# Kernel tuning notes

Hardware: AMD Instinct MI355X
Metric: run time of the kernel (lower is better)

The kernel has to match this reference:

```python
import jax, jax.numpy as jnp
import numpy as np

B, D, E = 8, 256, 2048
H, DK, DV = 8, 32, 32
LN_EPS = 1e-6
MASK_FILL = -1e9


def setup_inputs() -> dict:
    key = jax.random.key(0)
    ks = jax.random.split(key, 6)
    scale = 1.0 / np.sqrt(D)
    x = jax.random.normal(ks[0], (B, D, E), dtype=jnp.float32)
    mask = jax.random.randint(ks[1], (B, E, E), 0, 2).astype(bool)
    w_qs = jax.random.normal(ks[2], (D, H * DK), dtype=jnp.float32) * scale
    w_ks = jax.random.normal(ks[3], (D, H * DK), dtype=jnp.float32) * scale
    w_vs = jax.random.normal(ks[4], (D, H * DV), dtype=jnp.float32) * scale
    w_fc = jax.random.normal(ks[5], (H * DV, D), dtype=jnp.float32) * scale
    ln_gamma = jnp.ones((D,), dtype=jnp.float32)
    ln_beta = jnp.zeros((D,), dtype=jnp.float32)
    return {"x": x, "mask": mask, "w_qs": w_qs, "w_ks": w_ks,
            "w_vs": w_vs, "w_fc": w_fc, "ln_gamma": ln_gamma, "ln_beta": ln_beta}


def reference(x, mask, w_qs, w_ks, w_vs, w_fc, ln_gamma, ln_beta):
    # x: [B, D, E] -> s: [B, E, D]  (edges as sequence, features as d_model)
    s = jnp.transpose(x, (0, 2, 1))
    residual = s
    # LayerNorm applied to queries only (as in the original MultiHeadAttention)
    mu = jnp.mean(s, axis=-1, keepdims=True)
    var = jnp.mean((s - mu) ** 2, axis=-1, keepdims=True)
    q_in = (s - mu) * jax.lax.rsqrt(var + LN_EPS) * ln_gamma + ln_beta
    # projections -> [B, H, E, dk/dv]
    q = (q_in @ w_qs).reshape(B, E, H, DK).transpose(0, 2, 1, 3)
    k = (s @ w_ks).reshape(B, E, H, DK).transpose(0, 2, 1, 3)
    v = (s @ w_vs).reshape(B, E, H, DV).transpose(0, 2, 1, 3)
    temperature = jnp.sqrt(jnp.asarray(DK, dtype=q.dtype))
    scores = jnp.einsum('bhqd,bhkd->bhqk', q / temperature, k)
    scores = jnp.where(mask[:, None, :, :], scores, MASK_FILL)
    attn = jax.nn.softmax(scores, axis=-1)  # [B, H, E, E]
    out = jnp.einsum('bhqk,bhkd->bhqd', attn, v)
    out = out.transpose(0, 2, 1, 3).reshape(B, E, H * DV)
    out = out @ w_fc + residual  # dropout is identity in eval mode
    x_out = jnp.transpose(out, (0, 2, 1))  # back to [B, D, E]
    # attention-per-edge diagnostic (no gradient in original: attn.detach())
    attn_d = jax.lax.stop_gradient(attn)
    m = mask[:, None, :, :].astype(attn.dtype)  # [B, 1, E, E]
    attn_per_edge = jnp.sum(attn_d * m, axis=(1, 2)) / jnp.sum(m, axis=(1, 2))
    return (x_out, attn, attn_per_edge)
```

## Files before the change

kernel.cpp:

```cpp
#include <hip/hip_runtime.h>
#include <hip/hip_fp16.h>

#define TB 8
#define TD 256
#define TE 2048
#define TH 8

typedef _Float16 h8 __attribute__((ext_vector_type(8)));
typedef _Float16 h2_t __attribute__((ext_vector_type(2)));
typedef float    f4 __attribute__((ext_vector_type(4)));

static __device__ __forceinline__ unsigned int packh2(float a, float b){
  __half2 h = __floats2half2_rn(a, b);
  return __builtin_bit_cast(unsigned int, h);
}
static __device__ __forceinline__ h2_t u2h(unsigned int u){
  return __builtin_bit_cast(h2_t, u);
}
static __device__ __forceinline__ float fdot2f(h2_t a, h2_t b, float c){
#if __has_builtin(__builtin_amdgcn_fdot2)
  return __builtin_amdgcn_fdot2(a, b, c, false);
#else
  return c + (float)a[0]*(float)b[0] + (float)a[1]*(float)b[1];
#endif
}

__global__ __launch_bounds__(256) void k_pack(const unsigned int* __restrict__ mraw,
                       unsigned int* __restrict__ packed, float* __restrict__ num){
  __shared__ int oks;
  const int t = threadIdx.x;
  if(t == 0) oks = 1;
  __syncthreads();
  int ok = 1;
  for(int i=t; i<4096; i+=256) if(mraw[i] > 1u) ok = 0;
  if(!ok) atomicAnd(&oks, 0);
  __syncthreads();
  const int isInt = oks;

  const int row = blockIdx.x*4 + (t >> 6);
  const int w = t & 63;
  const size_t base = (size_t)row*TE + (size_t)w*32;
  unsigned int bits = 0;
  if(isInt){
    const unsigned int* p = mraw + base;
    #pragma unroll
    for(int j=0;j<32;j++) bits |= (p[j] & 1u) << j;
  } else {
    const unsigned char* p = (const unsigned char*)mraw + base;
    #pragma unroll
    for(int j=0;j<32;j++) bits |= (unsigned int)(p[j] != 0) << j;
  }
  packed[(size_t)row*64 + w] = bits;
  if(blockIdx.x < 64) num[blockIdx.x*256 + t] = 0.f;
}

__global__ __launch_bounds__(256) void k_denom(const unsigned int* __restrict__ packed,
                        float* __restrict__ denom){
  const int b = blockIdx.z;
  const int k = blockIdx.x*256 + threadIdx.x;
  const int q0 = blockIdx.y*64;
  const unsigned int* p = packed + ((size_t)b*TE + q0)*64 + (k >> 5);
  const unsigned sh = k & 31;
  int cnt = 0;
  #pragma unroll 8
  for(int q=0;q<64;q++) cnt += (p[(size_t)q*64] >> sh) & 1u;
  atomicAdd(&denom[b*TE + k], (float)cnt);
}

__global__ __launch_bounds__(256) void k_wpack(
    const float* __restrict__ wqs, const float* __restrict__ wks,
    const float* __restrict__ wvs, const float* __restrict__ wfc,
    unsigned int* __restrict__ wq2, unsigned int* __restrict__ wk2,
    unsigned int* __restrict__ wv2, unsigned int* __restrict__ wf2){
  const int idx = blockIdx.x*256 + threadIdx.x;
  const int m = idx >> 15;
  const int r = idx & 32767;
  const int dd2 = r >> 8, cc = r & 255;
  const float* src = (m==0) ? wqs : (m==1) ? wks : (m==2) ? wvs : wfc;
  unsigned int* dst = (m==0) ? wq2 : (m==1) ? wk2 : (m==2) ? wv2 : wf2;
  dst[dd2*256 + cc] = packh2(src[(2*dd2)*256 + cc], src[(2*dd2+1)*256 + cc]);
}

__global__ __launch_bounds__(256) void k_qkv(
    const float* __restrict__ x,
    const unsigned int* __restrict__ wq2, const unsigned int* __restrict__ wk2,
    const unsigned int* __restrict__ wv2,
    const float* __restrict__ gamma, const float* __restrict__ beta,
    _Float16* __restrict__ qh, _Float16* __restrict__ kh, _Float16* __restrict__ vt){
  __shared__ float xs[16][260];
  __shared__ unsigned int qi2[16][132];
  __shared__ unsigned int xs2[16][132];
  __shared__ float mu_s[16], rs_s[16];
  const int t = threadIdx.x;
  const int b = blockIdx.y;
  const int e0 = blockIdx.x*16;

  for(int i=t;i<16*256;i+=256){
    int el = i & 15, dd = i >> 4;
    xs[el][dd] = x[((size_t)(b*TD + dd))*TE + e0 + el];
  }
  __syncthreads();
  {
    int row = t >> 4, j = t & 15;
    float s1=0.f, s2=0.f;
    #pragma unroll
    for(int i=0;i<16;i++){ float v = xs[row][j*16+i]; s1 += v; s2 += v*v; }
    #pragma unroll
    for(int off=1; off<16; off<<=1){ s1 += __shfl_xor(s1, off); s2 += __shfl_xor(s2, off); }
    if(j==0){
      float m = s1 * (1.f/256.f);
      float var = s2 * (1.f/256.f) - m*m;
      mu_s[row] = m;
      rs_s[row] = rsqrtf(var + 1e-6f);
    }
  }
  __syncthreads();
  for(int i=t;i<16*128;i+=256){
    int r = i >> 7, dd2 = i & 127;
    float x0 = xs[r][2*dd2], x1 = xs[r][2*dd2+1];
    xs2[r][dd2] = packh2(x0, x1);
    float q0v = (x0 - mu_s[r]) * rs_s[r] * gamma[2*dd2]   + beta[2*dd2];
    float q1v = (x1 - mu_s[r]) * rs_s[r] * gamma[2*dd2+1] + beta[2*dd2+1];
    qi2[r][dd2] = packh2(q0v, q1v);
  }
  __syncthreads();

  const int c = t;
  float aq[16], ak[16], av[16];
  #pragma unroll
  for(int r=0;r<16;r++){ aq[r]=0.f; ak[r]=0.f; av[r]=0.f; }
  for(int dd2=0; dd2<128; dd2+=4){
    unsigned int wq[4], wk[4], wv[4];
    #pragma unroll
    for(int u=0;u<4;u++){
      wq[u] = wq2[(dd2+u)*256 + c];
      wk[u] = wk2[(dd2+u)*256 + c];
      wv[u] = wv2[(dd2+u)*256 + c];
    }
    #pragma unroll
    for(int r=0;r<16;r++){
      uint4 a4 = *(const uint4*)&qi2[r][dd2];
      uint4 s4 = *(const uint4*)&xs2[r][dd2];
      aq[r] = fdot2f(u2h(a4.x), u2h(wq[0]), aq[r]);
      aq[r] = fdot2f(u2h(a4.y), u2h(wq[1]), aq[r]);
      aq[r] = fdot2f(u2h(a4.z), u2h(wq[2]), aq[r]);
      aq[r] = fdot2f(u2h(a4.w), u2h(wq[3]), aq[r]);
      ak[r] = fdot2f(u2h(s4.x), u2h(wk[0]), ak[r]);
      ak[r] = fdot2f(u2h(s4.y), u2h(wk[1]), ak[r]);
      ak[r] = fdot2f(u2h(s4.z), u2h(wk[2]), ak[r]);
      ak[r] = fdot2f(u2h(s4.w), u2h(wk[3]), ak[r]);
      av[r] = fdot2f(u2h(s4.x), u2h(wv[0]), av[r]);
      av[r] = fdot2f(u2h(s4.y), u2h(wv[1]), av[r]);
      av[r] = fdot2f(u2h(s4.z), u2h(wv[2]), av[r]);
      av[r] = fdot2f(u2h(s4.w), u2h(wv[3]), av[r]);
    }
  }
  const int hh = c >> 5, d2 = c & 31;
  const float scl = 0.17677669529663687f;
  const size_t hb = ((size_t)(b*TH + hh))*TE;
  #pragma unroll
  for(int r=0;r<16;r++){
    size_t idx = (hb + e0 + r)*32 + d2;
    qh[idx] = (_Float16)(aq[r]*scl);
    kh[idx] = (_Float16)(ak[r]);
  }
  unsigned int pk[8];
  #pragma unroll
  for(int i2=0;i2<8;i2++) pk[i2] = packh2(av[2*i2], av[2*i2+1]);
  const int jj = (e0 >> 4) & 1;
  _Float16* vr = vt + ((size_t)(b*TH + hh)*32 + d2)*TE + (e0 & ~31) + 4*jj;
  #pragma unroll
  for(int gp=0; gp<4; gp++){
    uint2 w2v; w2v.x = pk[2*gp]; w2v.y = pk[2*gp+1];
    *(uint2*)&vr[8*gp] = w2v;
  }
}

__global__ __launch_bounds__(256) void k_attn(
    const _Float16* __restrict__ qh, const _Float16* __restrict__ kh, const _Float16* __restrict__ vt,
    const unsigned int* __restrict__ packed,
    float* __restrict__ attn, _Float16* __restrict__ owh, float* __restrict__ num){
  __shared__ unsigned int mb[64][66];
  __shared__ float num_s[TE];
  __shared__ __align__(16) f4 S4[4][272];

  const int t = threadIdx.x;
  int bid = blockIdx.x;
  bid = (bid & 7) * 256 + (bid >> 3);
  const int qt = bid & 31;
  const int bhid = bid >> 5;
  const int h = bhid & 7, b = bhid >> 3;
  const size_t bh = (size_t)bhid * TE;
  const _Float16* Qg = qh + bh*32;
  const _Float16* Kg = kh + bh*32;
  const _Float16* Vg = vt + bh*32;
  const int q0 = qt*64;

  const int wid = t >> 6, l = t & 63, g = l >> 4, c = l & 15;
  const int qr = wid*16 + c;
  const f4 f4z = {0.f, 0.f, 0.f, 0.f};

  for(int i=t;i<TE;i+=256) num_s[i] = 0.f;
  for(int i=t;i<64*64;i+=256){
    int r = i >> 6, w = i & 63;
    mb[r][w] = packed[((size_t)b*TE + q0 + r)*64 + w];
  }
  __syncthreads();

  const h8 qf = *(const h8*)(Qg + (size_t)(q0 + qr)*32 + g*8);
  const unsigned int* mrow = mb[qr];

  float ll = 0.f;
  for(int kt=0; kt<32; ++kt){
    h8 kf[4];
    #pragma unroll
    for(int j=0;j<4;j++) kf[j] = *(const h8*)(Kg + (size_t)(kt*64 + j*16 + c)*32 + g*8);
    f4 s[4];
    #pragma unroll
    for(int j=0;j<4;j++) s[j] = __builtin_amdgcn_mfma_f32_16x16x32_f16(kf[j], qf, f4z, 0, 0, 0);
    const unsigned mw0 = mrow[kt*2], mw1 = mrow[kt*2+1];
    #pragma unroll
    for(int j=0;j<4;j++){
      const unsigned mw = (j>>1) ? mw1 : mw0;
      #pragma unroll
      for(int r=0;r<4;r++){
        float sv = ((mw >> ((j&1)*16 + 4*g + r)) & 1u) ? s[j][r] : -1e9f;
        ll += __expf(sv);
      }
    }
  }
  ll += __shfl_xor(ll, 16);
  ll += __shfl_xor(ll, 32);
  const float rl = 1.f / ll;

  f4 oacc[2] = {f4z, f4z};
  f4* Sw = S4[wid];
  float* abase = attn + (bh + q0 + wid*16)*TE;
  for(int kt=0; kt<32; ++kt){
    h8 kf[4];
    #pragma unroll
    for(int j=0;j<4;j++) kf[j] = *(const h8*)(Kg + (size_t)(kt*64 + j*16 + c)*32 + g*8);
    f4 s[4];
    #pragma unroll
    for(int j=0;j<4;j++) s[j] = __builtin_amdgcn_mfma_f32_16x16x32_f16(kf[j], qf, f4z, 0, 0, 0);
    const unsigned mw0 = mrow[kt*2], mw1 = mrow[kt*2+1];
    unsigned int pk[4][2];
    #pragma unroll
    for(int j=0;j<4;j++){
      const unsigned mw = (j>>1) ? mw1 : mw0;
      f4 p;
      #pragma unroll
      for(int r=0;r<4;r++){
        float sv = ((mw >> ((j&1)*16 + 4*g + r)) & 1u) ? s[j][r] : -1e9f;
        p[r] = __expf(sv) * rl;
      }
      Sw[c*17 + 4*j + g] = p;
      pk[j][0] = packh2(p[0], p[1]);
      pk[j][1] = packh2(p[2], p[3]);
    }
    #pragma unroll
    for(int kc=0;kc<2;kc++){
      uint4 pu = {pk[2*kc][0], pk[2*kc][1], pk[2*kc+1][0], pk[2*kc+1][1]};
      h8 pf = __builtin_bit_cast(h8, pu);
      #pragma unroll
      for(int du=0;du<2;du++){
        h8 vf = *(const h8*)(Vg + (size_t)(du*16 + c)*TE + kt*64 + kc*32 + g*8);
        oacc[du] = __builtin_amdgcn_mfma_f32_16x16x32_f16(vf, pf, oacc[du], 0, 0, 0);
      }
    }
    f4 v[4];
    #pragma unroll
    for(int u=0;u<4;u++) v[u] = Sw[(u*4+g)*17 + c];
    #pragma unroll
    for(int u=0;u<4;u++)
      __builtin_nontemporal_store(v[u], (f4*)(abase + (size_t)(u*4+g)*TE + kt*64 + c*4));
    f4 a = v[0] + v[1] + v[2] + v[3];
    #pragma unroll
    for(int q=0;q<4;q++){ a[q] += __shfl_xor(a[q], 16); a[q] += __shfl_xor(a[q], 32); }
    if(l < 16){
      float* np = &num_s[kt*64 + c*4];
      atomicAdd(np+0, a[0]); atomicAdd(np+1, a[1]);
      atomicAdd(np+2, a[2]); atomicAdd(np+3, a[3]);
    }
  }

  #pragma unroll
  for(int du=0;du<2;du++){
    uint2 ov;
    ov.x = packh2(oacc[du][0], oacc[du][1]);
    ov.y = packh2(oacc[du][2], oacc[du][3]);
    *(uint2*)&owh[((size_t)b*TE + q0 + qr)*256 + h*32 + du*16 + 4*g] = ov;
  }
  __syncthreads();
  for(int i=t;i<TE;i+=256) atomicAdd(&num[(size_t)b*TE + i], num_s[i]);
}

__global__ __launch_bounds__(256) void k_fc(
    const _Float16* __restrict__ owh, const unsigned int* __restrict__ wf2,
    const float* __restrict__ x, float* __restrict__ xout){
  __shared__ unsigned int os2[16][132];
  __shared__ float xt[16][260];
  const int t = threadIdx.x;
  const int b = blockIdx.y;
  const int e0 = blockIdx.x * 16;
  const unsigned int* ow2 = (const unsigned int*)owh;
  for(int i=t;i<16*128;i+=256){
    int r = i >> 7, dd2 = i & 127;
    os2[r][dd2] = ow2[((size_t)b*TE + e0 + r)*128 + dd2];
  }
  for(int i=t;i<4096;i+=256){
    int el = i & 15, dd = i >> 4;
    xt[el][dd] = x[((size_t)(b*TD + dd))*TE + e0 + el];
  }
  __syncthreads();
  const int c = t;
  float f[16];
  #pragma unroll
  for(int r=0;r<16;r++) f[r] = 0.f;
  for(int dd2=0; dd2<128; dd2+=4){
    unsigned int wf[4];
    #pragma unroll
    for(int u=0;u<4;u++) wf[u] = wf2[(dd2+u)*256 + c];
    #pragma unroll
    for(int r=0;r<16;r++){
      uint4 o4 = *(const uint4*)&os2[r][dd2];
      f[r] = fdot2f(u2h(o4.x), u2h(wf[0]), f[r]);
      f[r] = fdot2f(u2h(o4.y), u2h(wf[1]), f[r]);
      f[r] = fdot2f(u2h(o4.z), u2h(wf[2]), f[r]);
      f[r] = fdot2f(u2h(o4.w), u2h(wf[3]), f[r]);
    }
  }
  __syncthreads();
  #pragma unroll
  for(int r=0;r<16;r++) xt[r][c] = f[r] + xt[r][c];
  __syncthreads();
  for(int i=t;i<4096;i+=256){
    int el = i & 15, dd = i >> 4;
    xout[((size_t)(b*TD + dd))*TE + e0 + el] = xt[el][dd];
  }
}

__global__ void k_edge(const float* __restrict__ num, const float* __restrict__ denom,
                       float* __restrict__ pe){
  int idx = blockIdx.x*256 + threadIdx.x;
  pe[idx] = num[idx] / (8.f * denom[idx]);
}

extern "C" void kernel_launch(void* const* d_in, const int* in_sizes, int n_in,
                              void* d_out, int out_size, void* d_ws, size_t ws_size,
                              hipStream_t stream){
  const float* x   = (const float*)d_in[0];
  const unsigned int* mraw = (const unsigned int*)d_in[1];
  const float* wqs = (const float*)d_in[2];
  const float* wks = (const float*)d_in[3];
  const float* wvs = (const float*)d_in[4];
  const float* wfc = (const float*)d_in[5];
  const float* gamma = (const float*)d_in[6];
  const float* beta  = (const float*)d_in[7];

  float* xout = (float*)d_out;
  float* attn = xout + (size_t)TB*TD*TE;
  float* pe   = attn + (size_t)TB*TH*TE*TE;

  const size_t SZ = (size_t)TB*TH*TE*32;
  _Float16* qhp = (_Float16*)((char*)d_ws + 256);
  _Float16* khp = qhp + SZ;
  _Float16* vtp = khp + SZ;
  _Float16* owh = vtp + SZ;
  unsigned int* packed = (unsigned int*)(owh + SZ);
  float* num   = (float*)(packed + (size_t)TB*TE*64);
  float* denom = num + (size_t)TB*TE;
  unsigned int* wq2 = (unsigned int*)(denom + (size_t)TB*TE);
  unsigned int* wk2 = wq2 + 32768;
  unsigned int* wv2 = wk2 + 32768;
  unsigned int* wf2 = wv2 + 32768;

  hipMemsetAsync(denom, 0, (size_t)TB*TE*sizeof(float), stream);
  k_wpack<<<512, 256, 0, stream>>>(wqs, wks, wvs, wfc, wq2, wk2, wv2, wf2);
  k_pack<<<TB*TE/4, 256, 0, stream>>>(mraw, packed, num);
  k_denom<<<dim3(TE/256, TE/64, TB), 256, 0, stream>>>(packed, denom);
  k_qkv<<<dim3(TE/16, TB), 256, 0, stream>>>(x, wq2, wk2, wv2, gamma, beta, qhp, khp, vtp);
  k_attn<<<TB*TH*TE/64, 256, 0, stream>>>(qhp, khp, vtp, packed, attn, owh, num);
  k_fc<<<dim3(TE/16, TB), 256, 0, stream>>>(owh, wf2, x, xout);
  k_edge<<<TB*TE/256, 256, 0, stream>>>(num, denom, pe);
}
```

Baseline: 413.5 us.

## Use MFMA for QKV and FC projections, fold log2e into Q scale, drop mask LDS staging

The QKV and output projections move from fdot2 scalar loops to 16x16x32 f16 MFMA, using transposed fp16 weight buffers built by the weight-pack kernel. The Q scale now includes log2(e), so the attention kernel can use exp2f instead of __expf. The attention kernel also reads mask bits straight from global memory as uint2 rather than staging them in shared memory. The projections were a small share of total time, so the benefit is limited, and the scattered per-element V stores may be less efficient than before.

Result: slower. 447.0 us (+8.1%).

```diff
diff --git a/kernel.cpp b/kernel.cpp
--- a/kernel.cpp
+++ b/kernel.cpp
@@ -1,5 +1,6 @@
 #include <hip/hip_runtime.h>
 #include <hip/hip_fp16.h>
+#include <math.h>
 
 #define TB 8
 #define TD 256
@@ -7,22 +8,11 @@
 #define TH 8
 
 typedef _Float16 h8 __attribute__((ext_vector_type(8)));
-typedef _Float16 h2_t __attribute__((ext_vector_type(2)));
 typedef float    f4 __attribute__((ext_vector_type(4)));
 
 static __device__ __forceinline__ unsigned int packh2(float a, float b){
   __half2 h = __floats2half2_rn(a, b);
   return __builtin_bit_cast(unsigned int, h);
-}
-static __device__ __forceinline__ h2_t u2h(unsigned int u){
-  return __builtin_bit_cast(h2_t, u);
-}
-static __device__ __forceinline__ float fdot2f(h2_t a, h2_t b, float c){
-#if __has_builtin(__builtin_amdgcn_fdot2)
-  return __builtin_amdgcn_fdot2(a, b, c, false);
-#else
-  return c + (float)a[0]*(float)b[0] + (float)a[1]*(float)b[1];
-#endif
 }
 
 __global__ __launch_bounds__(256) void k_pack(const unsigned int* __restrict__ mraw,
@@ -70,26 +60,22 @@
 __global__ __launch_bounds__(256) void k_wpack(
     const float* __restrict__ wqs, const float* __restrict__ wks,
     const float* __restrict__ wvs, const float* __restrict__ wfc,
-    unsigned int* __restrict__ wq2, unsigned int* __restrict__ wk2,
-    unsigned int* __restrict__ wv2, unsigned int* __restrict__ wf2){
-  const int idx = blockIdx.x*256 + threadIdx.x;
-  const int m = idx >> 15;
-  const int r = idx & 32767;
-  const int dd2 = r >> 8, cc = r & 255;
-  const float* src = (m==0) ? wqs : (m==1) ? wks : (m==2) ? wvs : wfc;
-  unsigned int* dst = (m==0) ? wq2 : (m==1) ? wk2 : (m==2) ? wv2 : wf2;
-  dst[dd2*256 + cc] = packh2(src[(2*dd2)*256 + cc], src[(2*dd2+1)*256 + cc]);
+    _Float16* __restrict__ qkvT, _Float16* __restrict__ fcT){
+  const int n = blockIdx.x;
+  const int k = threadIdx.x;
+  if(n < 256)      qkvT[(size_t)n*256 + k] = (_Float16)wqs[(size_t)k*256 + n];
+  else if(n < 512) qkvT[(size_t)n*256 + k] = (_Float16)wks[(size_t)k*256 + (n-256)];
+  else if(n < 768) qkvT[(size_t)n*256 + k] = (_Float16)wvs[(size_t)k*256 + (n-512)];
+  else             fcT[(size_t)(n-768)*256 + k] = (_Float16)wfc[(size_t)k*256 + (n-768)];
 }
 
 __global__ __launch_bounds__(256) void k_qkv(
-    const float* __restrict__ x,
-    const unsigned int* __restrict__ wq2, const unsigned int* __restrict__ wk2,
-    const unsigned int* __restrict__ wv2,
+    const float* __restrict__ x, const _Float16* __restrict__ qkvT,
     const float* __restrict__ gamma, const float* __restrict__ beta,
     _Float16* __restrict__ qh, _Float16* __restrict__ kh, _Float16* __restrict__ vt){
   __shared__ float xs[16][260];
-  __shared__ unsigned int qi2[16][132];
-  __shared__ unsigned int xs2[16][132];
+  __shared__ __align__(16) _Float16 xh[16][264];
+  __shared__ __align__(16) _Float16 qn[16][264];
   __shared__ float mu_s[16], rs_s[16];
   const int t = threadIdx.x;
   const int b = blockIdx.y;
@@ -115,64 +101,69 @@
     }
   }
   __syncthreads();
-  for(int i=t;i<16*128;i+=256){
-    int r = i >> 7, dd2 = i & 127;
-    float x0 = xs[r][2*dd2], x1 = xs[r][2*dd2+1];
-    xs2[r][dd2] = packh2(x0, x1);
-    float q0v = (x0 - mu_s[r]) * rs_s[r] * gamma[2*dd2]   + beta[2*dd2];
-    float q1v = (x1 - mu_s[r]) * rs_s[r] * gamma[2*dd2+1] + beta[2*dd2+1];
-    qi2[r][dd2] = packh2(q0v, q1v);
-  }
-  __syncthreads();
-
-  const int c = t;
-  float aq[16], ak[16], av[16];
-  #pragma unroll
-  for(int r=0;r<16;r++){ aq[r]=0.f; ak[r]=0.f; av[r]=0.f; }
-  for(int dd2=0; dd2<128; dd2+=4){
-    unsigned int wq[4], wk[4], wv[4];
-    #pragma unroll
-    for(int u=0;u<4;u++){
-      wq[u] = wq2[(dd2+u)*256 + c];
-      wk[u] = wk2[(dd2+u)*256 + c];
-      wv[u] = wv2[(dd2+u)*256 + c];
-    }
-    #pragma unroll
-    for(int r=0;r<16;r++){
-      uint4 a4 = *(const uint4*)&qi2[r][dd2];
-      uint4 s4 = *(const uint4*)&xs2[r][dd2];
-      aq[r] = fdot2f(u2h(a4.x), u2h(wq[0]), aq[r]);
-      aq[r] = fdot2f(u2h(a4.y), u2h(wq[1]), aq[r]);
-      aq[r] = fdot2f(u2h(a4.z), u2h(wq[2]), aq[r]);
-      aq[r] = fdot2f(u2h(a4.w), u2h(wq[3]), aq[r]);
-      ak[r] = fdot2f(u2h(s4.x), u2h(wk[0]), ak[r]);
-      ak[r] = fdot2f(u2h(s4.y), u2h(wk[1]), ak[r]);
-      ak[r] = fdot2f(u2h(s4.z), u2h(wk[2]), ak[r]);
-      ak[r] = fdot2f(u2h(s4.w), u2h(wk[3]), ak[r]);
-      av[r] = fdot2f(u2h(s4.x), u2h(wv[0]), av[r]);
-      av[r] = fdot2f(u2h(s4.y), u2h(wv[1]), av[r]);
-      av[r] = fdot2f(u2h(s4.z), u2h(wv[2]), av[r]);
-      av[r] = fdot2f(u2h(s4.w), u2h(wv[3]), av[r]);
-    }
-  }
-  const int hh = c >> 5, d2 = c & 31;
-  const float scl = 0.17677669529663687f;
-  const size_t hb = ((size_t)(b*TH + hh))*TE;
-  #pragma unroll
-  for(int r=0;r<16;r++){
-    size_t idx = (hb + e0 + r)*32 + d2;
-    qh[idx] = (_Float16)(aq[r]*scl);
-    kh[idx] = (_Float16)(ak[r]);
-  }
-  unsigned int pk[8];
-  #pragma unroll
-  for(int i2=0;i2<8;i2++) pk[i2] = packh2(av[2*i2], av[2*i2+1]);
+  for(int i=t;i<16*256;i+=256){
+    int r = i >> 8, dd = i & 255;
+    float xv = xs[r][dd];
+    xh[r][dd] = (_Float16)xv;
+    qn[r][dd] = (_Float16)((xv - mu_s[r]) * rs_s[r] * gamma[dd] + beta[dd]);
+  }
+  __syncthreads();
+
+  const int w = t >> 6, l = t & 63, g = l >> 4, c = l & 15;
+  const f4 f4z = {0.f,0.f,0.f,0.f};
+  const float sclq = 0.17677669529663687f * 1.44269504088896f;
+  h8 af[8];
+
+  #pragma unroll
+  for(int kk=0;kk<8;kk++) af[kk] = *(const h8*)&qn[c][kk*32 + g*8];
+  #pragma unroll
+  for(int i=0;i<4;i++){
+    const int n0 = (4*w+i)*16;
+    f4 acc = f4z;
+    #pragma unroll
+    for(int kk=0;kk<8;kk++){
+      h8 bf = *(const h8*)(qkvT + (size_t)(n0 + c)*256 + kk*32 + g*8);
+      acc = __builtin_amdgcn_mfma_f32_16x16x32_f16(bf, af[kk], acc, 0, 0, 0);
+    }
+    const int d0 = n0 + 4*g, hh = d0 >> 5, d2 = d0 & 31;
+    uint2 ov;
+    ov.x = packh2(acc[0]*sclq, acc[1]*sclq);
+    ov.y = packh2(acc[2]*sclq, acc[3]*sclq);
+    *(uint2*)&qh[((size_t)(b*TH+hh)*TE + e0 + c)*32 + d2] = ov;
+  }
+  #pragma unroll
+  for(int kk=0;kk<8;kk++) af[kk] = *(const h8*)&xh[c][kk*32 + g*8];
+  #pragma unroll
+  for(int i=0;i<4;i++){
+    const int n0 = (4*w+i)*16;
+    f4 acc = f4z;
+    #pragma unroll
+    for(int kk=0;kk<8;kk++){
+      h8 bf = *(const h8*)(qkvT + (size_t)(256 + n0 + c)*256 + kk*32 + g*8);
+      acc = __builtin_amdgcn_mfma_f32_16x16x32_f16(bf, af[kk], acc, 0, 0, 0);
+    }
+    const int d0 = n0 + 4*g, hh = d0 >> 5, d2 = d0 & 31;
+    uint2 ov;
+    ov.x = packh2(acc[0], acc[1]);
+    ov.y = packh2(acc[2], acc[3]);
+    *(uint2*)&kh[((size_t)(b*TH+hh)*TE + e0 + c)*32 + d2] = ov;
+  }
   const int jj = (e0 >> 4) & 1;
-  _Float16* vr = vt + ((size_t)(b*TH + hh)*32 + d2)*TE + (e0 & ~31) + 4*jj;
-  #pragma unroll
-  for(int gp=0; gp<4; gp++){
-    uint2 w2v; w2v.x = pk[2*gp]; w2v.y = pk[2*gp+1];
-    *(uint2*)&vr[8*gp] = w2v;
+  const int ep = (e0 & ~31) + 8*(c>>2) + 4*jj + (c&3);
+  #pragma unroll
+  for(int i=0;i<4;i++){
+    const int n0 = (4*w+i)*16;
+    f4 acc = f4z;
+    #pragma unroll
+    for(int kk=0;kk<8;kk++){
+      h8 bf = *(const h8*)(qkvT + (size_t)(512 + n0 + c)*256 + kk*32 + g*8);
+      acc = __builtin_amdgcn_mfma_f32_16x16x32_f16(bf, af[kk], acc, 0, 0, 0);
+    }
+    #pragma unroll
+    for(int r=0;r<4;r++){
+      const int d = n0 + 4*g + r;
+      vt[((size_t)(b*TH + (d>>5))*32 + (d&31))*TE + ep] = (_Float16)acc[r];
+    }
   }
 }
 
@@ -180,7 +171,6 @@
     const _Float16* __restrict__ qh, const _Float16* __restrict__ kh, const _Float16* __restrict__ vt,
     const unsigned int* __restrict__ packed,
     float* __restrict__ attn, _Float16* __restrict__ owh, float* __restrict__ num){
-  __shared__ unsigned int mb[64][66];
   __shared__ float num_s[TE];
   __shared__ __align__(16) f4 S4[4][272];
 
@@ -201,14 +191,10 @@
   const f4 f4z = {0.f, 0.f, 0.f, 0.f};
 
   for(int i=t;i<TE;i+=256) num_s[i] = 0.f;
-  for(int i=t;i<64*64;i+=256){
-    int r = i >> 6, w = i & 63;
-    mb[r][w] = packed[((size_t)b*TE + q0 + r)*64 + w];
-  }
   __syncthreads();
 
   const h8 qf = *(const h8*)(Qg + (size_t)(q0 + qr)*32 + g*8);
-  const unsigned int* mrow = mb[qr];
+  const uint2* mrow2 = (const uint2*)(packed + ((size_t)b*TE + q0 + qr)*64);
 
   float ll = 0.f;
   for(int kt=0; kt<32; ++kt){
@@ -218,14 +204,14 @@
     f4 s[4];
     #pragma unroll
     for(int j=0;j<4;j++) s[j] = __builtin_amdgcn_mfma_f32_16x16x32_f16(kf[j], qf, f4z, 0, 0, 0);
-    const unsigned mw0 = mrow[kt*2], mw1 = mrow[kt*2+1];
+    const uint2 mw2 = mrow2[kt];
     #pragma unroll
     for(int j=0;j<4;j++){
-      const unsigned mw = (j>>1) ? mw1 : mw0;
+      const unsigned mw = (j>>1) ? mw2.y : mw2.x;
       #pragma unroll
       for(int r=0;r<4;r++){
         float sv = ((mw >> ((j&1)*16 + 4*g + r)) & 1u) ? s[j][r] : -1e9f;
-        ll += __expf(sv);
+        ll += exp2f(sv);
       }
     }
   }
@@ -243,16 +229,16 @@
     f4 s[4];
     #pragma unroll
     for(int j=0;j<4;j++) s[j] = __builtin_amdgcn_mfma_f32_16x16x32_f16(kf[j], qf, f4z, 0, 0, 0);
-    const unsigned mw0 = mrow[kt*2], mw1 = mrow[kt*2+1];
+    const uint2 mw2 = mrow2[kt];
     unsigned int pk[4][2];
     #pragma unroll
     for(int j=0;j<4;j++){
-      const unsigned mw = (j>>1) ? mw1 : mw0;
+      const unsigned mw = (j>>1) ? mw2.y : mw2.x;
       f4 p;
       #pragma unroll
       for(int r=0;r<4;r++){
         float sv = ((mw >> ((j&1)*16 + 4*g + r)) & 1u) ? s[j][r] : -1e9f;
-        p[r] = __expf(sv) * rl;
+        p[r] = exp2f(sv) * rl;
       }
       Sw[c*17 + 4*j + g] = p;
       pk[j][0] = packh2(p[0], p[1]);
@@ -296,43 +282,40 @@
 }
 
 __global__ __launch_bounds__(256) void k_fc(
-    const _Float16* __restrict__ owh, const unsigned int* __restrict__ wf2,
+    const _Float16* __restrict__ owh, const _Float16* __restrict__ fcT,
     const float* __restrict__ x, float* __restrict__ xout){
-  __shared__ unsigned int os2[16][132];
   __shared__ float xt[16][260];
   const int t = threadIdx.x;
   const int b = blockIdx.y;
   const int e0 = blockIdx.x * 16;
-  const unsigned int* ow2 = (const unsigned int*)owh;
-  for(int i=t;i<16*128;i+=256){
-    int r = i >> 7, dd2 = i & 127;
-    os2[r][dd2] = ow2[((size_t)b*TE + e0 + r)*128 + dd2];
-  }
   for(int i=t;i<4096;i+=256){
     int el = i & 15, dd = i >> 4;
     xt[el][dd] = x[((size_t)(b*TD + dd))*TE + e0 + el];
   }
-  __syncthreads();
-  const int c = t;
-  float f[16];
-  #pragma unroll
-  for(int r=0;r<16;r++) f[r] = 0.f;
-  for(int dd2=0; dd2<128; dd2+=4){
-    unsigned int wf[4];
-    #pragma unroll
-    for(int u=0;u<4;u++) wf[u] = wf2[(dd2+u)*256 + c];
-    #pragma unroll
-    for(int r=0;r<16;r++){
-      uint4 o4 = *(const uint4*)&os2[r][dd2];
-      f[r] = fdot2f(u2h(o4.x), u2h(wf[0]), f[r]);
-      f[r] = fdot2f(u2h(o4.y), u2h(wf[1]), f[r]);
-      f[r] = fdot2f(u2h(o4.z), u2h(wf[2]), f[r]);
-      f[r] = fdot2f(u2h(o4.w), u2h(wf[3]), f[r]);
-    }
-  }
-  __syncthreads();
-  #pragma unroll
-  for(int r=0;r<16;r++) xt[r][c] = f[r] + xt[r][c];
+  const int w = t >> 6, l = t & 63, g = l >> 4, c = l & 15;
+  h8 af[8];
+  #pragma unroll
+  for(int kk=0;kk<8;kk++)
+    af[kk] = *(const h8*)(owh + ((size_t)b*TE + e0 + c)*256 + kk*32 + g*8);
+  f4 accs[4];
+  #pragma unroll
+  for(int i=0;i<4;i++){
+    const int n0 = w*64 + i*16;
+    f4 acc = {0.f,0.f,0.f,0.f};
+    #pragma unroll
+    for(int kk=0;kk<8;kk++){
+      h8 bf = *(const h8*)(fcT + (size_t)(n0 + c)*256 + kk*32 + g*8);
+      acc = __builtin_amdgcn_mfma_f32_16x16x32_f16(bf, af[kk], acc, 0, 0, 0);
+    }
+    accs[i] = acc;
+  }
+  __syncthreads();
+  #pragma unroll
+  for(int i=0;i<4;i++){
+    const int n0 = w*64 + i*16 + 4*g;
+    #pragma unroll
+    for(int r=0;r<4;r++) xt[c][n0+r] += accs[i][r];
+  }
   __syncthreads();
   for(int i=t;i<4096;i+=256){
     int el = i & 15, dd = i >> 4;
@@ -370,17 +353,15 @@
   unsigned int* packed = (unsigned int*)(owh + SZ);
   float* num   = (float*)(packed + (size_t)TB*TE*64);
   float* denom = num + (size_t)TB*TE;
-  unsigned int* wq2 = (unsigned int*)(denom + (size_t)TB*TE);
-  unsigned int* wk2 = wq2 + 32768;
-  unsigned int* wv2 = wk2 + 32768;
-  unsigned int* wf2 = wv2 + 32768;
+  _Float16* qkvT = (_Float16*)(denom + (size_t)TB*TE);
+  _Float16* fcT  = qkvT + 768*256;
 
   hipMemsetAsync(denom, 0, (size_t)TB*TE*sizeof(float), stream);
-  k_wpack<<<512, 256, 0, stream>>>(wqs, wks, wvs, wfc, wq2, wk2, wv2, wf2);
+  k_wpack<<<1024, 256, 0, stream>>>(wqs, wks, wvs, wfc, qkvT, fcT);
   k_pack<<<TB*TE/4, 256, 0, stream>>>(mraw, packed, num);
   k_denom<<<dim3(TE/256, TE/64, TB), 256, 0, stream>>>(packed, denom);
-  k_qkv<<<dim3(TE/16, TB), 256, 0, stream>>>(x, wq2, wk2, wv2, gamma, beta, qhp, khp, vtp);
+  k_qkv<<<dim3(TE/16, TB), 256, 0, stream>>>(x, qkvT, gamma, beta, qhp, khp, vtp);
   k_attn<<<TB*TH*TE/64, 256, 0, stream>>>(qhp, khp, vtp, packed, attn, owh, num);
-  k_fc<<<dim3(TE/16, TB), 256, 0, stream>>>(owh, wf2, x, xout);
+  k_fc<<<dim3(TE/16, TB), 256, 0, stream>>>(owh, fcT, x, xout);
   k_edge<<<TB*TE/256, 256, 0, stream>>>(num, denom, pe);
 }
```
